# Optimization experiments

Measured on AMD Instinct MI355X. Metric: run time of the kernel, lower is better.

## Reference

```python
import jax, jax.numpy as jnp
import numpy as np

N_NODES = 50000
N_EDGES = 800000
IN_DIM = 100

def setup_inputs() -> dict:
    key = jax.random.key(0)
    ks = jax.random.split(key, 12)
    nf = jax.random.normal(ks[0], (3, IN_DIM), dtype=jnp.float32)
    tid = jax.random.randint(ks[1], (N_NODES,), 0, 4)
    xr = jax.random.normal(ks[2], (N_NODES, IN_DIM), dtype=jnp.float32)
    # nodes of type 0/1/2 get exact prototype rows; type 3 ('edge') gets random rows
    x = jnp.where((tid < 3)[:, None], nf[jnp.clip(tid, 0, 2)], xr)
    edge_index = jax.random.randint(ks[3], (2, N_EDGES), 0, N_NODES, dtype=jnp.int32)
    def w(k, fi, fo):
        return jax.random.normal(k, (fi, fo), dtype=jnp.float32) * (1.0 / np.sqrt(fi))
    return {
        'x': x, 'node_feature': nf, 'edge_index': edge_index,
        'W1': w(ks[4], 100, 512), 'b1': jnp.zeros((512,), jnp.float32),
        'W2': w(ks[5], 512, 256), 'b2': jnp.zeros((256,), jnp.float32),
        'W3': w(ks[6], 256, 128), 'b3': jnp.zeros((128,), jnp.float32),
        'W4': w(ks[7], 128, 200), 'b4': jnp.zeros((200,), jnp.float32),
    }

def _gcn_forward(x, edge_index, W1, b1, W2, b2, W3, b3, W4, b4):
    N = x.shape[0]
    loop = jnp.arange(N, dtype=edge_index.dtype)
    src = jnp.concatenate([edge_index[0], loop])
    dst = jnp.concatenate([edge_index[1], loop])
    deg = jax.ops.segment_sum(jnp.ones_like(src, dtype=x.dtype), dst, num_segments=N)
    dinv = jnp.where(deg > 0, jax.lax.rsqrt(deg), 0.0)
    norm = dinv[src] * dinv[dst]  # symmetric GCN normalization with self-loops
    def gcn(h, W, b):
        h = h @ W
        agg = jax.ops.segment_sum(h[src] * norm[:, None], dst, num_segments=N)
        return agg + b
    out = jax.nn.relu(gcn(x, W1, b1))
    out = jax.nn.relu(gcn(out, W2, b2))
    out = jax.nn.relu(gcn(out, W3, b3))
    out = jax.nn.relu(gcn(out, W4, b4))
    return out

def _cat_mean(x, out, node_feature):
    # Vectorized replacement of the per-node python loop: output slot order is
    # init(nf0)->0, accept(nf2)->1, edge(other)->2, common(nf1)->3, matching the
    # original append order when all groups are nonempty.
    eq = jnp.all(x[:, None, :] == node_feature[None, :, :], axis=-1)  # [N,3]
    group = jnp.where(eq[:, 0], 0, jnp.where(eq[:, 1], 3, jnp.where(eq[:, 2], 1, 2)))
    sums = jax.ops.segment_sum(out, group, num_segments=4)            # [4,D]
    cnt = jax.ops.segment_sum(jnp.ones((x.shape[0],), out.dtype), group, num_segments=4)
    means = jnp.where(cnt[:, None] > 0, sums / jnp.maximum(cnt, 1.0)[:, None], 0.0)
    return means.reshape(1, -1)  # [1, 4*D]

def reference(x, node_feature, edge_index, W1, b1, W2, b2, W3, b3, W4, b4):
    out = _gcn_forward(x, edge_index, W1, b1, W2, b2, W3, b3, W4, b4)
    return _cat_mean(x, out, node_feature)
```

## Files before the change

kernel.cpp:

```cpp
#include <hip/hip_runtime.h>
#include <stdint.h>

typedef __attribute__((ext_vector_type(8))) short bf16x8;
typedef __attribute__((ext_vector_type(4))) float f32x4;

__device__ __forceinline__ float bf2f(ushort h) {
    union { uint u; float f; } v; v.u = ((uint)h) << 16; return v.f;
}
__device__ __forceinline__ ushort f2bf(float f) {
    union { float f; uint u; } v; v.f = f;
    uint u = v.u;
    return (ushort)((u + 0x7fffu + ((u >> 16) & 1u)) >> 16);
}

__device__ __forceinline__ void gll(const ushort* g, ushort* l) {
    __builtin_amdgcn_global_load_lds(
        (const __attribute__((address_space(1))) void*)g,
        (__attribute__((address_space(3))) void*)l, 16, 0, 0);
}


__device__ __forceinline__ void tr2_one(const float* __restrict__ W,
                                        ushort* __restrict__ WTh, ushort* __restrict__ WTl,
                                        int K, int Nc, int KP, int idx) {
    int n = idx / KP, k = idx % KP;
    float w = (n < Nc && k < K) ? W[(size_t)k * Nc + n] : 0.0f;
    ushort hi = f2bf(w);
    ushort lo = f2bf(w - bf2f(hi));
    WTh[idx] = hi;
    WTl[idx] = lo;
}

__global__ void k_init(const uint* __restrict__ xu, const uint* __restrict__ nfu,
                       ushort* __restrict__ xb, int* __restrict__ gid, int NN,
                       const int* __restrict__ dst, int E, int* __restrict__ deg,
                       const float* __restrict__ W1, const float* __restrict__ W2,
                       const float* __restrict__ W3, const float* __restrict__ W4,
                       ushort* __restrict__ WT1h, ushort* __restrict__ WT1l,
                       ushort* __restrict__ WT2h, ushort* __restrict__ WT2l,
                       ushort* __restrict__ WT3h, ushort* __restrict__ WT3l,
                       ushort* __restrict__ WT4h, ushort* __restrict__ WT4l,
                       int PB, int EB) {
    int b = blockIdx.x;
    if (b < PB) {
        int wid = b * 4 + (threadIdx.x >> 6);
        int lane = threadIdx.x & 63;
        if (wid >= NN) return;
        int c0 = lane * 2;
        uint w = 0u;
        int m0 = 1, m1 = 1, m2 = 1;
        if (c0 < 100) {
            uint2 xv = *(const uint2*)&xu[(size_t)wid * 100 + c0];
            uint2 a = *(const uint2*)&nfu[c0];
            uint2 bb = *(const uint2*)&nfu[100 + c0];
            uint2 c = *(const uint2*)&nfu[200 + c0];
            m0 = (xv.x == a.x) & (xv.y == a.y);
            m1 = (xv.x == bb.x) & (xv.y == bb.y);
            m2 = (xv.x == c.x) & (xv.y == c.y);
            w = (uint)f2bf(__uint_as_float(xv.x)) | ((uint)f2bf(__uint_as_float(xv.y)) << 16);
        }
        int e0 = __all(m0), e1 = __all(m1), e2 = __all(m2);
        *(uint*)&xb[(size_t)wid * 128 + c0] = w;
        if (lane == 0) gid[wid] = e0 ? 0 : (e1 ? 3 : (e2 ? 1 : 2));
    } else if (b < PB + EB) {
        int e = (b - PB) * 256 + threadIdx.x;
        if (e < E) atomicAdd(&deg[dst[e]], 1);
    } else {
        int idx = (b - PB - EB) * 256 + threadIdx.x;
        if (idx < 65536) tr2_one(W1, WT1h, WT1l, 100, 512, 128, idx);
        else if (idx < 196608) tr2_one(W2, WT2h, WT2l, 512, 256, 512, idx - 65536);
        else if (idx < 229376) tr2_one(W3, WT3h, WT3l, 256, 128, 256, idx - 196608);
        else if (idx < 262144) tr2_one(W4, WT4h, WT4l, 128, 200, 128, idx - 229376);
    }
}


__global__ void k_scanA(const int* __restrict__ deg, int* __restrict__ offs,
                        int* __restrict__ bsum, float* __restrict__ dinv,
                        const int* __restrict__ gid, int* __restrict__ gcnt, int NN) {
    __shared__ int lds[256];
    __shared__ int cnt4[4];
    int t = threadIdx.x;
    if (t < 4) cnt4[t] = 0;
    int i = blockIdx.x * 256 + t;
    int v = (i < NN) ? deg[i] : 0;
    if (i < NN) dinv[i] = 1.0f / sqrtf((float)(v + 1));
    lds[t] = v;
    __syncthreads();
    if (i < NN) atomicAdd(&cnt4[gid[i]], 1);
    for (int d = 1; d < 256; d <<= 1) {
        int u = (t >= d) ? lds[t - d] : 0;
        __syncthreads();
        lds[t] += u;
        __syncthreads();
    }
    if (i < NN) offs[i] = lds[t] - v;
    if (t == 255) bsum[blockIdx.x] = lds[255];
    __syncthreads();
    if (t < 4 && cnt4[t]) atomicAdd(&gcnt[t], cnt4[t]);
}


__global__ void k_fill(const int* __restrict__ src, const int* __restrict__ dst, int E,
                       const float* __restrict__ dinv, const int* __restrict__ offs,
                       const int* __restrict__ bsum,
                       int* __restrict__ cur, uint2* __restrict__ epk, int NN, int NB,
                       int* __restrict__ goffs) {
    __shared__ int sex[256];
    int t = threadIdx.x;
    int v = (t < NB) ? bsum[t] : 0;
    sex[t] = v;
    __syncthreads();
    for (int d = 1; d < 256; d <<= 1) {
        int u = (t >= d) ? sex[t - d] : 0;
        __syncthreads();
        sex[t] += u;
        __syncthreads();
    }
    int incl = sex[t];
    __syncthreads();
    sex[t] = incl - v;
    __syncthreads();
    int i = blockIdx.x * 256 + t;
    if (i < NN) goffs[i] = offs[i] + sex[i >> 8];
    if (i >= E) return;
    int s = src[i], d = dst[i];
    int p = offs[d] + sex[d >> 8] + atomicAdd(&cur[d], 1);
    epk[p] = make_uint2((uint)s, __float_as_uint(dinv[s] * dinv[d]));
}


__device__ __forceinline__ uint2 ldnt_u2(const uint2* p) {
    union { unsigned long long ll; uint2 v; } r;
    r.ll = __builtin_nontemporal_load((const unsigned long long*)p);
    return r.v;
}

__device__ __forceinline__ void fma2(uint u, float w, float& a0, float& a1) {
    union { uint u; float f; } lo, hi;
    lo.u = u << 16;
    hi.u = u & 0xffff0000u;
    a0 = fmaf(w, lo.f, a0);
    a1 = fmaf(w, hi.f, a1);
}

template <int UN, int LD>
__device__ __forceinline__ void agg_step(const ushort* __restrict__ Hc,
                                         const uint2* __restrict__ epk, int e,
                                         float& a0, float& a1) {
    uint2 q[UN];
#pragma unroll
    for (int i = 0; i < UN; ++i) q[i] = ldnt_u2(epk + e + i);
    uint u[UN];
#pragma unroll
    for (int i = 0; i < UN; ++i) u[i] = *(const uint*)(Hc + (size_t)q[i].x * LD);
#pragma unroll
    for (int i = 0; i < UN; ++i) fma2(u[i], __uint_as_float(q[i].y), a0, a1);
}

template <int LD, bool BR>
__global__ __launch_bounds__(256) void k_aggs(
        const ushort* __restrict__ H, ushort* __restrict__ outb,
        const float* __restrict__ dinv, const int* __restrict__ offs,
        const int* __restrict__ deg, const uint2* __restrict__ epk,
        const float* __restrict__ bias, int NN, int NNpad) {
    int wid = (int)((blockIdx.x * blockDim.x + threadIdx.x) >> 6);
    int lane = threadIdx.x & 63;
    if (wid >= NNpad) return;
    int c0 = lane * 2;
    ushort* op = outb + (size_t)wid * LD + c0;
    if (wid >= NN) {
        __builtin_nontemporal_store(0u, (uint*)op);
        return;
    }
    const ushort* Hc = H + c0;
    float a0 = 0.0f, a1 = 0.0f;
    {
        float di = dinv[wid];
        float sw = di * di;
        uint u = *(const uint*)(Hc + (size_t)wid * LD);
        fma2(u, sw, a0, a1);
    }
    int e = offs[wid];
    int end = e + deg[wid];
    for (; e + 8 <= end; e += 8) agg_step<8, LD>(Hc, epk, e, a0, a1);
    if (e + 4 <= end) { agg_step<4, LD>(Hc, epk, e, a0, a1); e += 4; }
    if (e + 2 <= end) { agg_step<2, LD>(Hc, epk, e, a0, a1); e += 2; }
    if (e < end) agg_step<1, LD>(Hc, epk, e, a0, a1);
    if (BR) {
        a0 = fmaxf(a0 + bias[c0], 0.0f);
        a1 = fmaxf(a1 + bias[c0 + 1], 0.0f);
    }
    uint w = (uint)f2bf(a0) | ((uint)f2bf(a1) << 16);
    __builtin_nontemporal_store(w, (uint*)op);
}


template <bool BR, int OUT>
__global__ __launch_bounds__(256) void k_gemm(
        const ushort* __restrict__ A,
        const ushort* __restrict__ Bh, const ushort* __restrict__ Bl,
        const float* __restrict__ bias,
        ushort* __restrict__ Cb,
        int Nc, int K, int tNb,
        const int* __restrict__ gid, float* __restrict__ gsum, int NN) {
    __shared__ union {
        ushort st[3][128 * 32];
        float epi[64 * 132];
    } sm;
    __shared__ int gcode[64];
    int bm = blockIdx.x / tNb, bn = blockIdx.x % tNb;
    int m0 = bm * 128, n0 = bn * 128;
    int wv = threadIdx.x >> 6, lane = threadIdx.x & 63;
    int l15 = lane & 15, quad = lane >> 4;
    const ushort* gsrc;
    ushort* ldst;
    int ng;
    if (wv == 0)      { gsrc = A  + (size_t)m0 * K;        ldst = sm.st[0];        ng = 4; }
    else if (wv == 1) { gsrc = A  + (size_t)(m0 + 64) * K; ldst = sm.st[0] + 2048; ng = 4; }
    else if (wv == 2) { gsrc = Bh + (size_t)n0 * K;        ldst = sm.st[1];        ng = 8; }
    else              { gsrc = Bl + (size_t)n0 * K;        ldst = sm.st[2];        ng = 8; }
    const ushort* gBase = gsrc + (size_t)(lane >> 2) * K + (lane & 3) * 8;
    int wm = (wv >> 1) * 64, wn = (wv & 1) * 64;
    const ushort* sA_ = sm.st[0];
    const ushort* sBh_ = sm.st[1];
    const ushort* sBl_ = sm.st[2];
    f32x4 acc[4][4] = {};
    for (int k0 = 0; k0 < K; k0 += 32) {
        for (int i = 0; i < ng; ++i)
            gll(gBase + (size_t)(16 * i) * K + k0, ldst + i * 512);
        __syncthreads();
        bf16x8 Af[4], Bfh[4], Bfl[4];
#pragma unroll
        for (int i = 0; i < 4; ++i) {
            int ra = (wm + 16 * i + l15) * 32 + quad * 8;
            int rb = (wn + 16 * i + l15) * 32 + quad * 8;
            Af[i]  = *(const bf16x8*)(sA_ + ra);
            Bfh[i] = *(const bf16x8*)(sBh_ + rb);
            Bfl[i] = *(const bf16x8*)(sBl_ + rb);
        }
#pragma unroll
        for (int mi = 0; mi < 4; ++mi)
#pragma unroll
            for (int ni = 0; ni < 4; ++ni) {
                acc[mi][ni] = __builtin_amdgcn_mfma_f32_16x16x32_bf16(Af[mi], Bfh[ni], acc[mi][ni], 0, 0, 0);
                acc[mi][ni] = __builtin_amdgcn_mfma_f32_16x16x32_bf16(Af[mi], Bfl[ni], acc[mi][ni], 0, 0, 0);
            }
        __syncthreads();
    }
    float bia[4] = {0.f, 0.f, 0.f, 0.f};
    if (BR) {
#pragma unroll
        for (int ni = 0; ni < 4; ++ni) {
            int col = n0 + wn + 16 * ni + l15;
            if (col < Nc) bia[ni] = bias[col];
        }
    }
    float* epi = sm.epi;
    int t = threadIdx.x;
    float s0 = 0.f, s1 = 0.f, s2 = 0.f, s3 = 0.f;
    int colR = t & 127, rg = t >> 7;
    for (int half = 0; half < 2; ++half) {
        if ((wv >> 1) == half) {
#pragma unroll
            for (int mi = 0; mi < 4; ++mi)
#pragma unroll
                for (int r = 0; r < 4; ++r) {
                    int rl = mi * 16 + quad * 4 + r;
#pragma unroll
                    for (int ni = 0; ni < 4; ++ni) {
                        float v = acc[mi][ni][r];
                        if (BR) v = fmaxf(v + bia[ni], 0.0f);
                        epi[rl * 132 + wn + ni * 16 + l15] = v;
                    }
                }
        }
        if (OUT == 2 && t < 64) {
            int grow = m0 + half * 64 + t;
            gcode[t] = (grow < NN) ? gid[grow] : -1;
        }
        __syncthreads();
        if (OUT == 2) {
#pragma unroll 4
            for (int r = 0; r < 32; ++r) {
                int row = rg * 32 + r;
                int g = gcode[row];
                float v = epi[row * 132 + colR];
                s0 += (g == 0) ? v : 0.f;
                s1 += (g == 1) ? v : 0.f;
                s2 += (g == 2) ? v : 0.f;
                s3 += (g == 3) ? v : 0.f;
            }
        } else {
#pragma unroll
            for (int j = 0; j < 16; ++j) {
                int e = (j * 256 + t) * 2;
                int rl = e >> 7, cl = e & 127;
                int grow = m0 + half * 64 + rl;
                int gcol = n0 + cl;
                float v0 = epi[rl * 132 + cl];
                float v1 = epi[rl * 132 + cl + 1];
                *(uint*)&Cb[(size_t)grow * Nc + gcol] = (uint)f2bf(v0) | ((uint)f2bf(v1) << 16);
            }
        }
        __syncthreads();
    }
    if (OUT == 2) {
        if (rg == 1) {
            epi[colR * 4 + 0] = s0; epi[colR * 4 + 1] = s1;
            epi[colR * 4 + 2] = s2; epi[colR * 4 + 3] = s3;
        }
        __syncthreads();
        if (rg == 0) {
            s0 += epi[colR * 4 + 0]; s1 += epi[colR * 4 + 1];
            s2 += epi[colR * 4 + 2]; s3 += epi[colR * 4 + 3];
            int gcol = n0 + colR;
            if (gcol < Nc) {
                atomicAdd(&gsum[0 * Nc + gcol], s0);
                atomicAdd(&gsum[1 * Nc + gcol], s1);
                atomicAdd(&gsum[2 * Nc + gcol], s2);
                atomicAdd(&gsum[3 * Nc + gcol], s3);
            }
        }
    }
}


__global__ void k_final(const float* __restrict__ gsum, const int* __restrict__ gcnt,
                        float* __restrict__ out) {
    int j = blockIdx.x * blockDim.x + threadIdx.x;
    if (j >= 800) return;
    int c = gcnt[j / 200];
    out[j] = (c > 0) ? gsum[j] / (float)c : 0.0f;
}


extern "C" void kernel_launch(void* const* d_in, const int* in_sizes, int n_in,
                              void* d_out, int out_size, void* d_ws, size_t ws_size,
                              hipStream_t stream) {
    const float* x  = (const float*)d_in[0];
    const float* nf = (const float*)d_in[1];
    const int* ei   = (const int*)d_in[2];
    const float* W1 = (const float*)d_in[3];
    const float* b1 = (const float*)d_in[4];
    const float* W2 = (const float*)d_in[5];
    const float* b2 = (const float*)d_in[6];
    const float* W3 = (const float*)d_in[7];
    const float* b3 = (const float*)d_in[8];
    const float* W4 = (const float*)d_in[9];
    const float* b4 = (const float*)d_in[10];
    float* out = (float*)d_out;

    const int NN = in_sizes[0] / 100;
    const int E  = in_sizes[2] / 2;
    const int MPAD = ((NN + 127) / 128) * 128;
    const int NB = (NN + 255) / 256;
    const int PB = (NN + 3) / 4;
    const int EB = (E + 255) / 256;
    const int TB = 1024;
    const int* src = ei;
    const int* dst = ei + E;

    char* p = (char*)d_ws;
    auto alloc = [&](size_t bytes) -> char* {
        char* r = p;
        p += (bytes + 255) & ~(size_t)255;
        return r;
    };
    char* zz = p;
    int*   deg  = (int*)alloc((size_t)NN * 4);
    int*   cur  = (int*)alloc((size_t)NN * 4);
    float* gsum = (float*)alloc(800 * 4);
    int*   gcnt = (int*)alloc(256);
    size_t zz_bytes = (size_t)(p - zz);
    float* dinv = (float*)alloc((size_t)NN * 4);
    int*   offs = (int*)alloc((size_t)NN * 4);
    int*   goffs = (int*)alloc((size_t)NN * 4);
    int*   bsum = (int*)alloc(1024);
    int*   gid  = (int*)alloc((size_t)NN * 4);
    uint2* epk  = (uint2*)alloc((size_t)E * 8);
    ushort* WT1h = (ushort*)alloc((size_t)512 * 128 * 2);
    ushort* WT1l = (ushort*)alloc((size_t)512 * 128 * 2);
    ushort* WT2h = (ushort*)alloc((size_t)256 * 512 * 2);
    ushort* WT2l = (ushort*)alloc((size_t)256 * 512 * 2);
    ushort* WT3h = (ushort*)alloc((size_t)128 * 256 * 2);
    ushort* WT3l = (ushort*)alloc((size_t)128 * 256 * 2);
    ushort* WT4h = (ushort*)alloc((size_t)256 * 128 * 2);
    ushort* WT4l = (ushort*)alloc((size_t)256 * 128 * 2);
    ushort* xb = (ushort*)alloc((size_t)NN * 128 * 2);
    ushort* P1 = (ushort*)alloc((size_t)MPAD * 128 * 2);
    ushort* H1 = (ushort*)alloc((size_t)MPAD * 512 * 2);
    ushort* T2 = (ushort*)alloc((size_t)MPAD * 256 * 2);
    ushort* H2 = (ushort*)alloc((size_t)MPAD * 256 * 2);
    ushort* T3 = (ushort*)alloc((size_t)MPAD * 128 * 2);
    ushort* H3 = (ushort*)alloc((size_t)MPAD * 128 * 2);
    ushort* P4 = (ushort*)alloc((size_t)MPAD * 128 * 2);

    hipMemsetAsync(zz, 0, zz_bytes, stream);

    k_init<<<PB + EB + TB, 256, 0, stream>>>(
        (const uint*)x, (const uint*)nf, xb, gid, NN, dst, E, deg,
        W1, W2, W3, W4, WT1h, WT1l, WT2h, WT2l, WT3h, WT3l, WT4h, WT4l, PB, EB);
    k_scanA<<<NB, 256, 0, stream>>>(deg, offs, bsum, dinv, gid, gcnt, NN);
    k_fill<<<EB, 256, 0, stream>>>(src, dst, E, dinv, offs, bsum, cur, epk, NN, NB, goffs);

    int aggBlocks = MPAD / 4;
    int mB = MPAD / 128;

    k_aggs<128, false><<<aggBlocks, 256, 0, stream>>>(xb, P1, dinv, goffs, deg, epk, nullptr, NN, MPAD);
    k_gemm<true, 1><<<mB * 4, 256, 0, stream>>>(P1, WT1h, WT1l, b1, H1, 512, 128, 4, nullptr, nullptr, 0);
    k_gemm<false, 1><<<mB * 2, 256, 0, stream>>>(H1, WT2h, WT2l, nullptr, T2, 256, 512, 2, nullptr, nullptr, 0);
    k_aggs<256, true><<<aggBlocks, 256, 0, stream>>>(T2, H2, dinv, goffs, deg, epk, b2, NN, MPAD);
    k_aggs<256, true><<<aggBlocks, 256, 0, stream>>>(T2 + 128, H2 + 128, dinv, goffs, deg, epk, b2 + 128, NN, MPAD);
    k_gemm<false, 1><<<mB * 1, 256, 0, stream>>>(H2, WT3h, WT3l, nullptr, T3, 128, 256, 1, nullptr, nullptr, 0);
    k_aggs<128, true><<<aggBlocks, 256, 0, stream>>>(T3, H3, dinv, goffs, deg, epk, b3, NN, MPAD);
    k_aggs<128, false><<<aggBlocks, 256, 0, stream>>>(H3, P4, dinv, goffs, deg, epk, nullptr, NN, MPAD);
    k_gemm<true, 2><<<mB * 2, 256, 0, stream>>>(P4, WT4h, WT4l, b4, nullptr, 200, 128, 2, gid, gsum, NN);

    k_final<<<4, 256, 0, stream>>>(gsum, gcnt, out);
}
```

Before: 462.8 us.

## Split aggregation edges across half-wavefronts and record CSR slots during degree count

The aggregation kernel now assigns each node's edge list to two 32-lane halves that each cover a 64-column slice, then combines the halves with a cross-lane shuffle. Column slices are spread across extra blocks, and the two 128-column layer-2 launches are merged into one. The degree-count atomic now returns each edge's slot, so the CSR fill no longer needs a second atomic pass over a cursor array, at the cost of an extra E-sized buffer. The fused init kernel is split into three separate launches, which adds launch overhead but removes the branching on block index.

```diff
diff --git a/kernel.cpp b/kernel.cpp
--- a/kernel.cpp
+++ b/kernel.cpp
@@ -17,6 +17,37 @@
     __builtin_amdgcn_global_load_lds(
         (const __attribute__((address_space(1))) void*)g,
         (__attribute__((address_space(3))) void*)l, 16, 0, 0);
+}
+
+
+__global__ void k_prep(const uint* __restrict__ xu, const uint* __restrict__ nfu,
+                       ushort* __restrict__ xb, int* __restrict__ gid, int NN) {
+    int wid = blockIdx.x * 4 + (threadIdx.x >> 6);
+    int lane = threadIdx.x & 63;
+    if (wid >= NN) return;
+    int c0 = lane * 2;
+    uint w = 0u;
+    int m0 = 1, m1 = 1, m2 = 1;
+    if (c0 < 100) {
+        uint2 xv = *(const uint2*)&xu[(size_t)wid * 100 + c0];
+        uint2 a = *(const uint2*)&nfu[c0];
+        uint2 bb = *(const uint2*)&nfu[100 + c0];
+        uint2 c = *(const uint2*)&nfu[200 + c0];
+        m0 = (xv.x == a.x) & (xv.y == a.y);
+        m1 = (xv.x == bb.x) & (xv.y == bb.y);
+        m2 = (xv.x == c.x) & (xv.y == c.y);
+        w = (uint)f2bf(__uint_as_float(xv.x)) | ((uint)f2bf(__uint_as_float(xv.y)) << 16);
+    }
+    int e0 = __all(m0), e1 = __all(m1), e2 = __all(m2);
+    *(uint*)&xb[(size_t)wid * 128 + c0] = w;
+    if (lane == 0) gid[wid] = e0 ? 0 : (e1 ? 3 : (e2 ? 1 : 2));
+}
+
+
+__global__ void k_deg(const int* __restrict__ dst, int E,
+                      int* __restrict__ deg, int* __restrict__ slot) {
+    int e = blockIdx.x * 256 + threadIdx.x;
+    if (e < E) slot[e] = atomicAdd(&deg[dst[e]], 1);
 }
 
 
@@ -31,47 +62,17 @@
     WTl[idx] = lo;
 }
 
-__global__ void k_init(const uint* __restrict__ xu, const uint* __restrict__ nfu,
-                       ushort* __restrict__ xb, int* __restrict__ gid, int NN,
-                       const int* __restrict__ dst, int E, int* __restrict__ deg,
-                       const float* __restrict__ W1, const float* __restrict__ W2,
-                       const float* __restrict__ W3, const float* __restrict__ W4,
-                       ushort* __restrict__ WT1h, ushort* __restrict__ WT1l,
-                       ushort* __restrict__ WT2h, ushort* __restrict__ WT2l,
-                       ushort* __restrict__ WT3h, ushort* __restrict__ WT3l,
-                       ushort* __restrict__ WT4h, ushort* __restrict__ WT4l,
-                       int PB, int EB) {
-    int b = blockIdx.x;
-    if (b < PB) {
-        int wid = b * 4 + (threadIdx.x >> 6);
-        int lane = threadIdx.x & 63;
-        if (wid >= NN) return;
-        int c0 = lane * 2;
-        uint w = 0u;
-        int m0 = 1, m1 = 1, m2 = 1;
-        if (c0 < 100) {
-            uint2 xv = *(const uint2*)&xu[(size_t)wid * 100 + c0];
-            uint2 a = *(const uint2*)&nfu[c0];
-            uint2 bb = *(const uint2*)&nfu[100 + c0];
-            uint2 c = *(const uint2*)&nfu[200 + c0];
-            m0 = (xv.x == a.x) & (xv.y == a.y);
-            m1 = (xv.x == bb.x) & (xv.y == bb.y);
-            m2 = (xv.x == c.x) & (xv.y == c.y);
-            w = (uint)f2bf(__uint_as_float(xv.x)) | ((uint)f2bf(__uint_as_float(xv.y)) << 16);
-        }
-        int e0 = __all(m0), e1 = __all(m1), e2 = __all(m2);
-        *(uint*)&xb[(size_t)wid * 128 + c0] = w;
-        if (lane == 0) gid[wid] = e0 ? 0 : (e1 ? 3 : (e2 ? 1 : 2));
-    } else if (b < PB + EB) {
-        int e = (b - PB) * 256 + threadIdx.x;
-        if (e < E) atomicAdd(&deg[dst[e]], 1);
-    } else {
-        int idx = (b - PB - EB) * 256 + threadIdx.x;
-        if (idx < 65536) tr2_one(W1, WT1h, WT1l, 100, 512, 128, idx);
-        else if (idx < 196608) tr2_one(W2, WT2h, WT2l, 512, 256, 512, idx - 65536);
-        else if (idx < 229376) tr2_one(W3, WT3h, WT3l, 256, 128, 256, idx - 196608);
-        else if (idx < 262144) tr2_one(W4, WT4h, WT4l, 128, 200, 128, idx - 229376);
-    }
+__global__ void k_wsplit(const float* __restrict__ W1, const float* __restrict__ W2,
+                         const float* __restrict__ W3, const float* __restrict__ W4,
+                         ushort* __restrict__ WT1h, ushort* __restrict__ WT1l,
+                         ushort* __restrict__ WT2h, ushort* __restrict__ WT2l,
+                         ushort* __restrict__ WT3h, ushort* __restrict__ WT3l,
+                         ushort* __restrict__ WT4h, ushort* __restrict__ WT4l) {
+    int idx = blockIdx.x * 256 + threadIdx.x;
+    if (idx < 65536) tr2_one(W1, WT1h, WT1l, 100, 512, 128, idx);
+    else if (idx < 196608) tr2_one(W2, WT2h, WT2l, 512, 256, 512, idx - 65536);
+    else if (idx < 229376) tr2_one(W3, WT3h, WT3l, 256, 128, 256, idx - 196608);
+    else if (idx < 262144) tr2_one(W4, WT4h, WT4l, 128, 200, 128, idx - 229376);
 }
 
 
@@ -101,10 +102,11 @@
 }
 
 
-__global__ void k_fill(const int* __restrict__ src, const int* __restrict__ dst, int E,
+__global__ void k_fill(const int* __restrict__ src, const int* __restrict__ dst,
+                       const int* __restrict__ slot, int E,
                        const float* __restrict__ dinv, const int* __restrict__ offs,
                        const int* __restrict__ bsum,
-                       int* __restrict__ cur, uint2* __restrict__ epk, int NN, int NB,
+                       uint2* __restrict__ epk, int NN, int NB,
                        int* __restrict__ goffs) {
     __shared__ int sex[256];
     int t = threadIdx.x;
@@ -125,7 +127,7 @@
     if (i < NN) goffs[i] = offs[i] + sex[i >> 8];
     if (i >= E) return;
     int s = src[i], d = dst[i];
-    int p = offs[d] + sex[d >> 8] + atomicAdd(&cur[d], 1);
+    int p = offs[d] + sex[d >> 8] + slot[i];
     epk[p] = make_uint2((uint)s, __float_as_uint(dinv[s] * dinv[d]));
 }
 
@@ -158,41 +160,51 @@
     for (int i = 0; i < UN; ++i) fma2(u[i], __uint_as_float(q[i].y), a0, a1);
 }
 
-template <int LD, bool BR>
+template <int LD, int NSL, bool BR>
 __global__ __launch_bounds__(256) void k_aggs(
         const ushort* __restrict__ H, ushort* __restrict__ outb,
         const float* __restrict__ dinv, const int* __restrict__ offs,
         const int* __restrict__ deg, const uint2* __restrict__ epk,
         const float* __restrict__ bias, int NN, int NNpad) {
-    int wid = (int)((blockIdx.x * blockDim.x + threadIdx.x) >> 6);
+    int slice = blockIdx.x % NSL;
+    int nb = blockIdx.x / NSL;
+    int wv = threadIdx.x >> 6;
+    int wid = nb * 4 + wv;
     int lane = threadIdx.x & 63;
+    int sl = lane & 31, half = lane >> 5;
     if (wid >= NNpad) return;
-    int c0 = lane * 2;
+    int c0 = slice * 64 + sl * 2;
     ushort* op = outb + (size_t)wid * LD + c0;
     if (wid >= NN) {
-        __builtin_nontemporal_store(0u, (uint*)op);
+        if (half == 0) __builtin_nontemporal_store(0u, (uint*)op);
         return;
     }
     const ushort* Hc = H + c0;
     float a0 = 0.0f, a1 = 0.0f;
-    {
+    if (half == 0) {
         float di = dinv[wid];
         float sw = di * di;
         uint u = *(const uint*)(Hc + (size_t)wid * LD);
         fma2(u, sw, a0, a1);
     }
-    int e = offs[wid];
-    int end = e + deg[wid];
+    int beg = offs[wid], d = deg[wid];
+    int d0 = (d + 1) >> 1;
+    int e = beg + half * d0;
+    int end = e + (half ? (d - d0) : d0);
     for (; e + 8 <= end; e += 8) agg_step<8, LD>(Hc, epk, e, a0, a1);
     if (e + 4 <= end) { agg_step<4, LD>(Hc, epk, e, a0, a1); e += 4; }
     if (e + 2 <= end) { agg_step<2, LD>(Hc, epk, e, a0, a1); e += 2; }
     if (e < end) agg_step<1, LD>(Hc, epk, e, a0, a1);
-    if (BR) {
-        a0 = fmaxf(a0 + bias[c0], 0.0f);
-        a1 = fmaxf(a1 + bias[c0 + 1], 0.0f);
-    }
-    uint w = (uint)f2bf(a0) | ((uint)f2bf(a1) << 16);
-    __builtin_nontemporal_store(w, (uint*)op);
+    a0 += __shfl_xor(a0, 32);
+    a1 += __shfl_xor(a1, 32);
+    if (half == 0) {
+        if (BR) {
+            a0 = fmaxf(a0 + bias[c0], 0.0f);
+            a1 = fmaxf(a1 + bias[c0 + 1], 0.0f);
+        }
+        uint w = (uint)f2bf(a0) | ((uint)f2bf(a1) << 16);
+        __builtin_nontemporal_store(w, (uint*)op);
+    }
 }
 
 
@@ -369,10 +381,10 @@
     };
     char* zz = p;
     int*   deg  = (int*)alloc((size_t)NN * 4);
-    int*   cur  = (int*)alloc((size_t)NN * 4);
     float* gsum = (float*)alloc(800 * 4);
     int*   gcnt = (int*)alloc(256);
     size_t zz_bytes = (size_t)(p - zz);
+    int*   slot = (int*)alloc((size_t)E * 4);
     float* dinv = (float*)alloc((size_t)NN * 4);
     int*   offs = (int*)alloc((size_t)NN * 4);
     int*   goffs = (int*)alloc((size_t)NN * 4);
@@ -398,23 +410,23 @@
 
     hipMemsetAsync(zz, 0, zz_bytes, stream);
 
-    k_init<<<PB + EB + TB, 256, 0, stream>>>(
-        (const uint*)x, (const uint*)nf, xb, gid, NN, dst, E, deg,
-        W1, W2, W3, W4, WT1h, WT1l, WT2h, WT2l, WT3h, WT3l, WT4h, WT4l, PB, EB);
+    k_prep<<<PB, 256, 0, stream>>>((const uint*)x, (const uint*)nf, xb, gid, NN);
+    k_deg<<<EB, 256, 0, stream>>>(dst, E, deg, slot);
+    k_wsplit<<<TB, 256, 0, stream>>>(W1, W2, W3, W4,
+        WT1h, WT1l, WT2h, WT2l, WT3h, WT3l, WT4h, WT4l);
     k_scanA<<<NB, 256, 0, stream>>>(deg, offs, bsum, dinv, gid, gcnt, NN);
-    k_fill<<<EB, 256, 0, stream>>>(src, dst, E, dinv, offs, bsum, cur, epk, NN, NB, goffs);
+    k_fill<<<EB, 256, 0, stream>>>(src, dst, slot, E, dinv, offs, bsum, epk, NN, NB, goffs);
 
     int aggBlocks = MPAD / 4;
     int mB = MPAD / 128;
 
-    k_aggs<128, false><<<aggBlocks, 256, 0, stream>>>(xb, P1, dinv, goffs, deg, epk, nullptr, NN, MPAD);
+    k_aggs<128, 2, false><<<aggBlocks * 2, 256, 0, stream>>>(xb, P1, dinv, goffs, deg, epk, nullptr, NN, MPAD);
     k_gemm<true, 1><<<mB * 4, 256, 0, stream>>>(P1, WT1h, WT1l, b1, H1, 512, 128, 4, nullptr, nullptr, 0);
     k_gemm<false, 1><<<mB * 2, 256, 0, stream>>>(H1, WT2h, WT2l, nullptr, T2, 256, 512, 2, nullptr, nullptr, 0);
-    k_aggs<256, true><<<aggBlocks, 256, 0, stream>>>(T2, H2, dinv, goffs, deg, epk, b2, NN, MPAD);
-    k_aggs<256, true><<<aggBlocks, 256, 0, stream>>>(T2 + 128, H2 + 128, dinv, goffs, deg, epk, b2 + 128, NN, MPAD);
+    k_aggs<256, 4, true><<<aggBlocks * 4, 256, 0, stream>>>(T2, H2, dinv, goffs, deg, epk, b2, NN, MPAD);
     k_gemm<false, 1><<<mB * 1, 256, 0, stream>>>(H2, WT3h, WT3l, nullptr, T3, 128, 256, 1, nullptr, nullptr, 0);
-    k_aggs<128, true><<<aggBlocks, 256, 0, stream>>>(T3, H3, dinv, goffs, deg, epk, b3, NN, MPAD);
-    k_aggs<128, false><<<aggBlocks, 256, 0, stream>>>(H3, P4, dinv, goffs, deg, epk, nullptr, NN, MPAD);
+    k_aggs<128, 2, true><<<aggBlocks * 2, 256, 0, stream>>>(T3, H3, dinv, goffs, deg, epk, b3, NN, MPAD);
+    k_aggs<128, 2, false><<<aggBlocks * 2, 256, 0, stream>>>(H3, P4, dinv, goffs, deg, epk, nullptr, NN, MPAD);
     k_gemm<true, 2><<<mB * 2, 256, 0, stream>>>(P4, WT4h, WT4l, b4, nullptr, 200, 128, 2, gid, gsum, NN);
 
     k_final<<<4, 256, 0, stream>>>(gsum, gcnt, out);
```

New measurement: 521.3 us. 1.13x slower.
